# Kernel tuning notes

Measured on AMD Instinct MI355X. Metric: run time of the kernel, lower is better.

Reference implementation:

```python
import jax, jax.numpy as jnp
import numpy as np
import math

F, M, C, OUT = 60, 600, 8, 18  # feature_size, max_samples, cluster_size, output_dim
B = 2048


def l2_normalize(x, axis):
    # matches tf.nn.l2_normalize (epsilon=1e-12)
    sq = jnp.sum(jnp.square(x), axis=axis, keepdims=True)
    return x * jax.lax.rsqrt(jnp.maximum(sq, 1e-12))


def setup_inputs() -> dict:
    key = jax.random.key(0)
    k = jax.random.split(key, 6)
    s1 = 1.0 / math.sqrt(F)
    s2 = 1.0 / math.sqrt(C)
    return {
        "reshaped_input": jax.random.normal(k[0], (B * M, F), dtype=jnp.float32),
        "cluster_weights": jax.random.normal(k[1], (F, C), dtype=jnp.float32) * s1,
        "covar_weights": jax.random.normal(k[2], (F, C), dtype=jnp.float32) * s1,
        "cluster_biases": jax.random.normal(k[3], (C,), dtype=jnp.float32) * s1,
        "cluster_weights2": jax.random.normal(k[4], (1, F, C), dtype=jnp.float32) * s1,
        "hidden1_weights": jax.random.normal(k[5], (2 * C * F, OUT), dtype=jnp.float32) * s2,
    }


def reference(reshaped_input, cluster_weights, covar_weights, cluster_biases,
              cluster_weights2, hidden1_weights):
    cw = jnp.square(covar_weights) + 1e-6                      # [F, C]

    act = reshaped_input @ cluster_weights + cluster_biases    # [B*M, C]
    act = jax.nn.softmax(act, axis=-1)
    act = act.reshape(-1, M, C)                                # [B, M, C]

    a_sum = jnp.sum(act, axis=-2, keepdims=True)               # [B, 1, C]
    a = a_sum * cluster_weights2                               # [B, F, C]

    x = reshaped_input.reshape(-1, M, F)                       # [B, M, F]

    fv1 = jnp.einsum('bmc,bmf->bfc', act, x)                   # [B, F, C]
    fv2 = jnp.einsum('bmc,bmf->bfc', act, jnp.square(x))       # [B, F, C]

    a2 = a_sum * jnp.square(cluster_weights2)                  # [B, F, C]
    b2 = fv1 * cluster_weights2                                # [B, F, C]

    fv2 = a2 + fv2 - 2.0 * b2
    fv2 = fv2 / jnp.square(cw)
    fv2 = fv2 - a_sum                                          # broadcast [B,1,C]
    fv2 = fv2.reshape(-1, C * F)
    fv2 = l2_normalize(fv2, axis=1)
    fv2 = l2_normalize(fv2, axis=1)  # second normalize as in original (idempotent)

    fv1 = (fv1 - a) / cw                                       # [B, F, C]
    fv1 = l2_normalize(fv1, axis=1)                            # per-cluster, along F
    fv1 = fv1.reshape(-1, C * F)
    fv1 = l2_normalize(fv1, axis=1)

    fv = jnp.concatenate([fv1, fv2], axis=1)                   # [B, 2*C*F]
    return fv @ hidden1_weights                                # [B, OUT]
```

## Files before the change

### kernel.cpp

```cpp
#include <hip/hip_runtime.h>

#define FDIM 60
#define MROW 600
#define CDIM 8
#define ODIM 18
#define CH   128
#define NCHUNK 5
#define BLK  512

typedef short bf16x8 __attribute__((ext_vector_type(8)));
typedef float f32x4  __attribute__((ext_vector_type(4)));

__device__ __forceinline__ unsigned int pk2(float lo, float hi) {
    unsigned int ul = __float_as_uint(lo), uh = __float_as_uint(hi);
    ul = (ul + 0x7fffu + ((ul >> 16) & 1u)) >> 16;
    uh = (uh + 0x7fffu + ((uh >> 16) & 1u)) & 0xffff0000u;
    return (ul & 0xffffu) | uh;
}
__device__ __forceinline__ short f2bf(float f) {
    unsigned int u = __float_as_uint(f);
    u = (u + 0x7fffu + ((u >> 16) & 1u)) >> 16;
    return (short)u;
}

__global__ void __launch_bounds__(BLK, 4) netfv_kernel(
    const float* __restrict__ x,
    const float* __restrict__ W,
    const float* __restrict__ covar,
    const float* __restrict__ bias,
    const float* __restrict__ cw2,
    const float* __restrict__ H,
    float* __restrict__ out)
{
    __shared__ __align__(16) short xsT1[64 * 136];
    __shared__ __align__(16) short xsT2[64 * 136];
    __shared__ __align__(16) short xsM [128 * 72];
    __shared__ __align__(16) short actT[16 * 136];
    __shared__ __align__(16) short WtB [16 * 72];
    __shared__ __align__(16) float fvbuf[1024];
    __shared__ __align__(16) float fvl[960];
    __shared__ float redA[64], redB[64];
    __shared__ float asuml[8], n1rs[8], n1c_s[8], n2c_s[8], scal[2];

    const int tid  = threadIdx.x;
    const int b    = blockIdx.x;
    const int lane = tid & 63;
    const int wv   = tid >> 6;
    const int mg   = tid >> 3;
    const int fs   = tid & 7;
    const int ln15 = lane & 15;
    const int quad = lane >> 4;
    const int fvsel = wv & 1;
    const int tile  = wv >> 1;

    const size_t rowbase = (size_t)b * (MROW * FDIM);
    const float* prow = x + rowbase + (size_t)(2 * mg) * FDIM + 8 * fs;

    float4 A0, A1, B0, B1;
    B0 = B1 = make_float4(0.f, 0.f, 0.f, 0.f);
    A0 = *(const float4*)prow;
    A1 = *(const float4*)(prow + FDIM);
    if (fs < 7) { B0 = *(const float4*)(prow + 4); B1 = *(const float4*)(prow + FDIM + 4); }

    if (tid < 512) {
        int c = tid >> 5, j = tid & 31;
        float v0 = (2 * j     < FDIM) ? W[(2 * j) * CDIM + c % CDIM]     : 0.f;
        float v1 = (2 * j + 1 < FDIM) ? W[(2 * j + 1) * CDIM + c % CDIM] : 0.f;
        if (c >= CDIM) { v0 = 0.f; v1 = 0.f; }
        ((unsigned int*)WtB)[c * 36 + j] = pk2(v0, v1);
    }
    {
        unsigned int* az = (unsigned int*)(actT + 8 * 136);
        for (int i = tid; i < 544; i += BLK) az[i] = 0u;
    }
    __syncthreads();

    const bf16x8 aw0 = *(const bf16x8*)(WtB + ln15 * 72 + quad * 8);
    const bf16x8 aw1 = *(const bf16x8*)(WtB + ln15 * 72 + 32 + quad * 8);
    const float4 lb  = *(const float4*)(bias + (quad & 1) * 4);

    f32x4 acc = {0.f, 0.f, 0.f, 0.f};
    float asum_acc[4] = {0.f, 0.f, 0.f, 0.f};
    const int mloc = wv * 16 + ln15;

    for (int ck = 0; ck < NCHUNK; ++ck) {
        const bool valid = (ck * CH + 2 * mg) < MROW;

        float4 nA0, nA1, nB0, nB1;
        nA0 = nA1 = nB0 = nB1 = make_float4(0.f, 0.f, 0.f, 0.f);
        if (ck + 1 < NCHUNK && ((ck + 1) * CH + 2 * mg) < MROW) {
            const float* pn = prow + (size_t)(ck + 1) * (CH * FDIM);
            nA0 = *(const float4*)pn;
            nA1 = *(const float4*)(pn + FDIM);
            if (fs < 7) { nB0 = *(const float4*)(pn + 4); nB1 = *(const float4*)(pn + FDIM + 4); }
        }

        if (valid) {
            float xv0[8] = {A0.x, A0.y, A0.z, A0.w, B0.x, B0.y, B0.z, B0.w};
            float xv1[8] = {A1.x, A1.y, A1.z, A1.w, B1.x, B1.y, B1.z, B1.w};
            {
                unsigned int q0 = pk2(xv0[0], xv0[1]), q1 = pk2(xv0[2], xv0[3]);
                unsigned int q2 = pk2(xv0[4], xv0[5]), q3 = pk2(xv0[6], xv0[7]);
                *(uint4*)(xsM + (2 * mg) * 72 + 8 * fs) = make_uint4(q0, q1, q2, q3);
                unsigned int s0 = pk2(xv1[0], xv1[1]), s1 = pk2(xv1[2], xv1[3]);
                unsigned int s2 = pk2(xv1[4], xv1[5]), s3 = pk2(xv1[6], xv1[7]);
                *(uint4*)(xsM + (2 * mg + 1) * 72 + 8 * fs) = make_uint4(s0, s1, s2, s3);
            }
            const int wbase = (((mg >> 2) ^ fs) << 2) + (mg & 3);
            #pragma unroll
            for (int i = 0; i < 8; ++i) {
                int woff = (8 * fs + i) * 68 + wbase;
                ((unsigned int*)xsT1)[woff] = pk2(xv0[i], xv1[i]);
                ((unsigned int*)xsT2)[woff] = pk2(xv0[i] * xv0[i], xv1[i] * xv1[i]);
            }
        }
        __syncthreads();

        {
            bf16x8 bv0 = *(const bf16x8*)(xsM + mloc * 72 + quad * 8);
            bf16x8 bv1 = *(const bf16x8*)(xsM + mloc * 72 + 32 + quad * 8);
            f32x4 lz = {0.f, 0.f, 0.f, 0.f};
            lz = __builtin_amdgcn_mfma_f32_16x16x32_bf16(aw0, bv0, lz, 0, 0, 0);
            lz = __builtin_amdgcn_mfma_f32_16x16x32_bf16(aw1, bv1, lz, 0, 0, 0);
            float L0 = lz[0] + lb.x, L1 = lz[1] + lb.y;
            float L2 = lz[2] + lb.z, L3 = lz[3] + lb.w;
            float mx = fmaxf(fmaxf(L0, L1), fmaxf(L2, L3));
            mx = fmaxf(mx, __shfl_xor(mx, 16));
            float e0 = __expf(L0 - mx), e1 = __expf(L1 - mx);
            float e2 = __expf(L2 - mx), e3 = __expf(L3 - mx);
            float s = e0 + e1 + e2 + e3;
            s += __shfl_xor(s, 16);
            float inv = __builtin_amdgcn_rcpf(s);
            const bool vm = (ck * CH + mloc) < MROW;
            if (quad < 2) {
                float a0 = vm ? e0 * inv : 0.f, a1v = vm ? e1 * inv : 0.f;
                float a2v = vm ? e2 * inv : 0.f, a3v = vm ? e3 * inv : 0.f;
                asum_acc[0] += a0;  asum_acc[1] += a1v;
                asum_acc[2] += a2v; asum_acc[3] += a3v;
                actT[(quad * 4 + 0) * 136 + mloc] = f2bf(a0);
                actT[(quad * 4 + 1) * 136 + mloc] = f2bf(a1v);
                actT[(quad * 4 + 2) * 136 + mloc] = f2bf(a2v);
                actT[(quad * 4 + 3) * 136 + mloc] = f2bf(a3v);
            }
        }
        __syncthreads();

        {
            const short* xsel = fvsel ? xsT2 : xsT1;
            const int f   = tile * 16 + ln15;
            const int fsw = f >> 3;
            #pragma unroll
            for (int ks = 0; ks < 4; ++ks) {
                bf16x8 av = *(const bf16x8*)(actT + ln15 * 136 + ks * 32 + quad * 8);
                int kblk = ks * 4 + quad;
                bf16x8 bv = *(const bf16x8*)(xsel + f * 136 + ((kblk ^ fsw) << 3));
                acc = __builtin_amdgcn_mfma_f32_16x16x32_bf16(av, bv, acc, 0, 0, 0);
            }
        }
        __syncthreads();
        A0 = nA0; A1 = nA1; B0 = nB0; B1 = nB1;
    }

    #pragma unroll
    for (int r = 0; r < 4; ++r) {
        float v = asum_acc[r];
        v += __shfl_xor(v, 1); v += __shfl_xor(v, 2);
        v += __shfl_xor(v, 4); v += __shfl_xor(v, 8);
        asum_acc[r] = v;
    }
    if (quad < 2 && ln15 == 0) {
        #pragma unroll
        for (int r = 0; r < 4; ++r) redA[wv * 8 + quad * 4 + r] = asum_acc[r];
    }
    __syncthreads();
    if (tid < 64) {
        float v = redA[tid];
        v += __shfl_down(v, 8); v += __shfl_down(v, 16); v += __shfl_down(v, 32);
        if (tid < 8) asuml[tid] = v;
    }
    if (quad < 2) {
        #pragma unroll
        for (int r = 0; r < 4; ++r)
            fvbuf[fvsel * 512 + (tile * 16 + ln15) * 8 + quad * 4 + r] = acc[r];
    }
    __syncthreads();

    float fv1v = 0.f, fv2v = 0.f;
    const int f_e = tid >> 3, c_e = tid & 7;
    if (tid < 480) {
        float fv1r = fvbuf[f_e * 8 + c_e];
        float fv2r = fvbuf[512 + f_e * 8 + c_e];
        float asv  = asuml[c_e];
        float cw2v = cw2[f_e * 8 + c_e];
        float cv   = covar[f_e * 8 + c_e];
        float cwv  = cv * cv + 1e-6f;
        float rcw  = 1.0f / cwv;
        fv1v = (fv1r - asv * cw2v) * rcw;
        fv2v = (fmaf(asv * cw2v, cw2v, fv2r) - 2.0f * fv1r * cw2v) * rcw * rcw - asv;
    }

    {
        float p1 = fv1v * fv1v, p2 = fv2v * fv2v;
        p1 += __shfl_down(p1, 8);  p2 += __shfl_down(p2, 8);
        p1 += __shfl_down(p1, 16); p2 += __shfl_down(p2, 16);
        p1 += __shfl_down(p1, 32); p2 += __shfl_down(p2, 32);
        if (lane < 8) { redA[wv * 8 + lane] = p1; redB[wv * 8 + lane] = p2; }
    }
    __syncthreads();
    if (tid < 64) {
        float q1 = redA[tid], q2 = redB[tid];
        q1 += __shfl_down(q1, 8);  q2 += __shfl_down(q2, 8);
        q1 += __shfl_down(q1, 16); q2 += __shfl_down(q2, 16);
        q1 += __shfl_down(q1, 32); q2 += __shfl_down(q2, 32);
        if (tid < 8) { n1c_s[tid] = q1; n2c_s[tid] = q2; }
    }
    __syncthreads();
    if (tid == 0) {
        float S1 = 0.f, S2 = 0.f;
        #pragma unroll
        for (int c = 0; c < 8; ++c) {
            float rs = rsqrtf(fmaxf(n1c_s[c], 1e-12f));
            n1rs[c] = rs;
            S1 += n1c_s[c] * rs * rs;
            S2 += n2c_s[c];
        }
        scal[0] = rsqrtf(fmaxf(S1, 1e-12f));
        scal[1] = rsqrtf(fmaxf(S2, 1e-12f));
    }
    __syncthreads();
    if (tid < 480) {
        fvl[f_e * 8 + c_e]       = fv1v * n1rs[c_e] * scal[0];
        fvl[480 + f_e * 8 + c_e] = fv2v * scal[1];
    }
    __syncthreads();

    for (int o = wv; o < ODIM; o += 8) {
        float sacc = 0.f;
        #pragma unroll 5
        for (int i = lane; i < 960; i += 64)
            sacc = fmaf(fvl[i], H[i * ODIM + o], sacc);
        sacc += __shfl_down(sacc, 32);
        sacc += __shfl_down(sacc, 16);
        sacc += __shfl_down(sacc, 8);
        sacc += __shfl_down(sacc, 4);
        sacc += __shfl_down(sacc, 2);
        sacc += __shfl_down(sacc, 1);
        if (lane == 0) out[(size_t)b * ODIM + o] = sacc;
    }
}

extern "C" void kernel_launch(void* const* d_in, const int* in_sizes, int n_in,
                              void* d_out, int out_size, void* d_ws, size_t ws_size,
                              hipStream_t stream) {
    const float* x     = (const float*)d_in[0];
    const float* W     = (const float*)d_in[1];
    const float* covar = (const float*)d_in[2];
    const float* bias  = (const float*)d_in[3];
    const float* cw2   = (const float*)d_in[4];
    const float* H     = (const float*)d_in[5];
    float* outp = (float*)d_out;

    const int Bn = in_sizes[0] / (MROW * FDIM);
    hipLaunchKernelGGL(netfv_kernel, dim3(Bn), dim3(BLK), 0, stream,
                       x, W, covar, bias, cw2, H, outp);
}
```

Before: 440.4 us.

## Load logits operand from global directly, drop xsM staging buffer and barrier

The row-major bf16 shared buffer used to feed the logit MFMA is removed. Each lane now reads its own row slice straight from global memory and packs it to bf16 in registers, which removes one __syncthreads per chunk and about 18KB of LDS. Launch bounds rise from 4 to 6 blocks per SM, and bf16 conversion now uses the HIP intrinsics. In exchange, each input row is read from global memory twice (probably served from cache) and register pressure may grow under the tighter launch bound.

```diff
diff --git a/kernel.cpp b/kernel.cpp
--- a/kernel.cpp
+++ b/kernel.cpp
@@ -1,4 +1,5 @@
 #include <hip/hip_runtime.h>
+#include <hip/hip_bf16.h>
 
 #define FDIM 60
 #define MROW 600
@@ -12,18 +13,19 @@
 typedef float f32x4  __attribute__((ext_vector_type(4)));
 
 __device__ __forceinline__ unsigned int pk2(float lo, float hi) {
-    unsigned int ul = __float_as_uint(lo), uh = __float_as_uint(hi);
-    ul = (ul + 0x7fffu + ((ul >> 16) & 1u)) >> 16;
-    uh = (uh + 0x7fffu + ((uh >> 16) & 1u)) & 0xffff0000u;
-    return (ul & 0xffffu) | uh;
+    __hip_bfloat162 h2 = __float22bfloat162_rn(make_float2(lo, hi));
+    unsigned int u;
+    __builtin_memcpy(&u, &h2, sizeof(u));
+    return u;
 }
 __device__ __forceinline__ short f2bf(float f) {
-    unsigned int u = __float_as_uint(f);
-    u = (u + 0x7fffu + ((u >> 16) & 1u)) >> 16;
-    return (short)u;
-}
-
-__global__ void __launch_bounds__(BLK, 4) netfv_kernel(
+    __hip_bfloat16 h = __float2bfloat16(f);
+    short s;
+    __builtin_memcpy(&s, &h, sizeof(s));
+    return s;
+}
+
+__global__ void __launch_bounds__(BLK, 6) netfv_kernel(
     const float* __restrict__ x,
     const float* __restrict__ W,
     const float* __restrict__ covar,
@@ -34,7 +36,6 @@
 {
     __shared__ __align__(16) short xsT1[64 * 136];
     __shared__ __align__(16) short xsT2[64 * 136];
-    __shared__ __align__(16) short xsM [128 * 72];
     __shared__ __align__(16) short actT[16 * 136];
     __shared__ __align__(16) short WtB [16 * 72];
     __shared__ __align__(16) float fvbuf[1024];
@@ -62,10 +63,10 @@
     A1 = *(const float4*)(prow + FDIM);
     if (fs < 7) { B0 = *(const float4*)(prow + 4); B1 = *(const float4*)(prow + FDIM + 4); }
 
-    if (tid < 512) {
+    {
         int c = tid >> 5, j = tid & 31;
-        float v0 = (2 * j     < FDIM) ? W[(2 * j) * CDIM + c % CDIM]     : 0.f;
-        float v1 = (2 * j + 1 < FDIM) ? W[(2 * j + 1) * CDIM + c % CDIM] : 0.f;
+        float v0 = (2 * j     < FDIM) ? W[(2 * j) * CDIM + (c & 7)]     : 0.f;
+        float v1 = (2 * j + 1 < FDIM) ? W[(2 * j + 1) * CDIM + (c & 7)] : 0.f;
         if (c >= CDIM) { v0 = 0.f; v1 = 0.f; }
         ((unsigned int*)WtB)[c * 36 + j] = pk2(v0, v1);
     }
@@ -95,17 +96,18 @@
             if (fs < 7) { nB0 = *(const float4*)(pn + 4); nB1 = *(const float4*)(pn + FDIM + 4); }
         }
 
+        const int grow = ck * CH + mloc;
+        const bool vm = grow < MROW;
+        const float* xr = x + rowbase + (size_t)(vm ? grow : (MROW - 1)) * FDIM;
+        float4 c0 = *(const float4*)(xr + quad * 8);
+        float4 c1 = *(const float4*)(xr + quad * 8 + 4);
+        float4 c2 = *(const float4*)(xr + 32 + quad * 8);
+        float4 c3 = (quad < 3) ? *(const float4*)(xr + 36 + quad * 8)
+                               : make_float4(0.f, 0.f, 0.f, 0.f);
+
         if (valid) {
             float xv0[8] = {A0.x, A0.y, A0.z, A0.w, B0.x, B0.y, B0.z, B0.w};
             float xv1[8] = {A1.x, A1.y, A1.z, A1.w, B1.x, B1.y, B1.z, B1.w};
-            {
-                unsigned int q0 = pk2(xv0[0], xv0[1]), q1 = pk2(xv0[2], xv0[3]);
-                unsigned int q2 = pk2(xv0[4], xv0[5]), q3 = pk2(xv0[6], xv0[7]);
-                *(uint4*)(xsM + (2 * mg) * 72 + 8 * fs) = make_uint4(q0, q1, q2, q3);
-                unsigned int s0 = pk2(xv1[0], xv1[1]), s1 = pk2(xv1[2], xv1[3]);
-                unsigned int s2 = pk2(xv1[4], xv1[5]), s3 = pk2(xv1[6], xv1[7]);
-                *(uint4*)(xsM + (2 * mg + 1) * 72 + 8 * fs) = make_uint4(s0, s1, s2, s3);
-            }
             const int wbase = (((mg >> 2) ^ fs) << 2) + (mg & 3);
             #pragma unroll
             for (int i = 0; i < 8; ++i) {
@@ -114,14 +116,16 @@
                 ((unsigned int*)xsT2)[woff] = pk2(xv0[i] * xv0[i], xv1[i] * xv1[i]);
             }
         }
-        __syncthreads();
 
         {
-            bf16x8 bv0 = *(const bf16x8*)(xsM + mloc * 72 + quad * 8);
-            bf16x8 bv1 = *(const bf16x8*)(xsM + mloc * 72 + 32 + quad * 8);
+            union { bf16x8 v; unsigned int u[4]; } Lo, Hi;
+            Lo.u[0] = pk2(c0.x, c0.y); Lo.u[1] = pk2(c0.z, c0.w);
+            Lo.u[2] = pk2(c1.x, c1.y); Lo.u[3] = pk2(c1.z, c1.w);
+            Hi.u[0] = pk2(c2.x, c2.y); Hi.u[1] = pk2(c2.z, c2.w);
+            Hi.u[2] = pk2(c3.x, c3.y); Hi.u[3] = pk2(c3.z, c3.w);
             f32x4 lz = {0.f, 0.f, 0.f, 0.f};
-            lz = __builtin_amdgcn_mfma_f32_16x16x32_bf16(aw0, bv0, lz, 0, 0, 0);
-            lz = __builtin_amdgcn_mfma_f32_16x16x32_bf16(aw1, bv1, lz, 0, 0, 0);
+            lz = __builtin_amdgcn_mfma_f32_16x16x32_bf16(aw0, Lo.v, lz, 0, 0, 0);
+            lz = __builtin_amdgcn_mfma_f32_16x16x32_bf16(aw1, Hi.v, lz, 0, 0, 0);
             float L0 = lz[0] + lb.x, L1 = lz[1] + lb.y;
             float L2 = lz[2] + lb.z, L3 = lz[3] + lb.w;
             float mx = fmaxf(fmaxf(L0, L1), fmaxf(L2, L3));
@@ -131,9 +135,8 @@
             float s = e0 + e1 + e2 + e3;
             s += __shfl_xor(s, 16);
             float inv = __builtin_amdgcn_rcpf(s);
-            const bool vm = (ck * CH + mloc) < MROW;
             if (quad < 2) {
-                float a0 = vm ? e0 * inv : 0.f, a1v = vm ? e1 * inv : 0.f;
+                float a0  = vm ? e0 * inv : 0.f, a1v = vm ? e1 * inv : 0.f;
                 float a2v = vm ? e2 * inv : 0.f, a3v = vm ? e3 * inv : 0.f;
                 asum_acc[0] += a0;  asum_acc[1] += a1v;
                 asum_acc[2] += a2v; asum_acc[3] += a3v;
```

Result: slower. 482.8 us (+9.6%).
